# Kernel tuning notes

Measured on AMD Instinct MI355X. Metric: run time of the kernel, lower is better.

The kernel has to match this reference:

```python
import jax, jax.numpy as jnp
import numpy as np

B_SZ, L, D_MODEL = 2, 1024, 1024
EXPAND, D_STATE, D_CONV = 2, 16, 4
D_INNER = D_MODEL * EXPAND
DT_RANK = max(D_MODEL // 16, 1)


def setup_inputs() -> dict:
    key = jax.random.key(0)
    ks = jax.random.split(key, 9)
    s = 0.02
    x = jax.random.normal(ks[0], (B_SZ, L, D_MODEL), jnp.float32)
    W_in = jax.random.normal(ks[1], (2 * D_INNER, D_MODEL), jnp.float32) * s
    conv_w = jax.random.normal(ks[2], (D_INNER, D_CONV), jnp.float32) * 0.1
    conv_b = jax.random.normal(ks[3], (D_INNER,), jnp.float32) * 0.01
    W_x = jax.random.normal(ks[4], (DT_RANK + 2 * D_STATE, D_INNER), jnp.float32) * s
    W_dt = jax.random.normal(ks[5], (D_INNER, DT_RANK), jnp.float32) * s
    b_dt = jax.random.normal(ks[6], (D_INNER,), jnp.float32) * 0.01
    A_log = jnp.log(jnp.broadcast_to(jnp.arange(1, D_STATE + 1, dtype=jnp.float32), (D_INNER, D_STATE)))
    D_param = jnp.ones((D_INNER,), jnp.float32)
    W_out = jax.random.normal(ks[7], (D_MODEL, D_INNER), jnp.float32) * s
    return {"x": x, "W_in": W_in, "conv_w": conv_w, "conv_b": conv_b,
            "W_x": W_x, "W_dt": W_dt, "b_dt": b_dt, "A_log": A_log,
            "D_param": D_param, "W_out": W_out}


def _mamba_fwd(x, W_in, conv_w, conv_b, W_x, W_dt, b_dt, A_log, D_param, W_out):
    # in-proj and gate split
    xz = jnp.einsum("bld,ed->ble", x, W_in)            # (B, L, 2*d_inner)
    x_ssm, z = jnp.split(xz, 2, axis=-1)
    # causal depthwise 1D conv (left pad d_conv-1 == torch pad-both + [:L])
    xc = x_ssm.transpose(0, 2, 1)                        # (B, d_inner, L)
    xc = jax.lax.conv_general_dilated(
        xc, conv_w[:, None, :], window_strides=(1,),
        padding=[(D_CONV - 1, 0)], feature_group_count=D_INNER,
        dimension_numbers=("NCH", "OIH", "NCH"))
    xc = xc + conv_b[None, :, None]
    x_ssm = jax.nn.silu(xc.transpose(0, 2, 1))           # (B, L, d_inner)
    # input-dependent dt, B, C
    dbc = jnp.einsum("bld,ed->ble", x_ssm, W_x)
    dt, B_sel, C_sel = jnp.split(dbc, [DT_RANK, DT_RANK + D_STATE], axis=-1)
    delta = jax.nn.softplus(jnp.einsum("blr,dr->bld", dt, W_dt) + b_dt)
    A = -jnp.exp(A_log)                                  # (d_inner, d_state)
    # discretization
    deltaA = jnp.exp(delta[..., None] * A)               # (B, L, d_inner, d_state)
    dBu = delta[..., None] * B_sel[:, :, None, :] * x_ssm[..., None]
    # linear recurrence h_t = deltaA_t * h_{t-1} + dBu_t via associative scan
    def comb(e1, e2):
        a1, b1 = e1
        a2, b2 = e2
        return (a1 * a2, a2 * b1 + b2)
    _, h = jax.lax.associative_scan(comb, (deltaA, dBu), axis=1)
    y = jnp.sum(h * C_sel[:, :, None, :], axis=-1)       # (B, L, d_inner)
    y = y + x_ssm * D_param
    y = y * jax.nn.silu(z)
    return jnp.einsum("ble,de->bld", y, W_out)


def reference(x, W_in, conv_w, conv_b, W_x, W_dt, b_dt, A_log, D_param, W_out):
    return _mamba_fwd(x, W_in, conv_w, conv_b, W_x, W_dt, b_dt, A_log, D_param, W_out)
```

## Files before the change

kernel.cpp:

```cpp
#include <hip/hip_runtime.h>
#include <hip/hip_bf16.h>

#define B_SZ   2
#define SEQ    1024
#define DMODEL 1024
#define DINNER 2048
#define DSTATE 16
#define DCONV  4
#define DTRANK 64
#define BLROWS (B_SZ*SEQ)
#define NCHUNK 32
#define TCHUNK (SEQ/NCHUNK)
#define NSLICE 16
#define LOG2E 1.44269504088896f

using floatx4 = __attribute__((ext_vector_type(4))) float;
using short8  = __attribute__((ext_vector_type(8))) short;
using us8     = __attribute__((ext_vector_type(8))) unsigned short;
using us4     = __attribute__((ext_vector_type(4))) unsigned short;

__device__ __forceinline__ float softplus_f(float x) {
    return fmaxf(x, 0.f) + log1pf(__expf(-fabsf(x)));
}
__device__ __forceinline__ float silu_f(float x) {
    return x / (1.f + __expf(-x));
}
__device__ __forceinline__ short bfs(float x) {
    union { __hip_bfloat16 h; short s; } u;
    u.h = __float2bfloat16(x);
    return u.s;
}
__device__ __forceinline__ float b2f(unsigned short s) {
    union { float f; unsigned u; } x;
    x.u = ((unsigned)s) << 16;
    return x.f;
}
__device__ __forceinline__ void gld16(const void* g, void* l) {
    __builtin_amdgcn_global_load_lds((const __attribute__((address_space(1))) void*)g,
                                     (__attribute__((address_space(3))) void*)l,
                                     16, 0, 0);
}
__device__ __forceinline__ void cast8(const float* src, unsigned short* dst, int i) {
    const float* p = src + (size_t)i*8;
    float4 a = *(const float4*)p, b = *(const float4*)(p+4);
    us8 o;
    o[0]=(unsigned short)bfs(a.x); o[1]=(unsigned short)bfs(a.y);
    o[2]=(unsigned short)bfs(a.z); o[3]=(unsigned short)bfs(a.w);
    o[4]=(unsigned short)bfs(b.x); o[5]=(unsigned short)bfs(b.y);
    o[6]=(unsigned short)bfs(b.z); o[7]=(unsigned short)bfs(b.w);
    *(us8*)(dst + (size_t)i*8) = o;
}

#define G0 (BLROWS*DMODEL/8)
#define G1 (2*DINNER*DMODEL/8)
#define G2 (96*DINNER/8)
#define G3 (DINNER*DTRANK/8)
#define G4 (DMODEL*DINNER/8)
#define GTOT (G0+G1+G2+G3+G4)
__global__ __launch_bounds__(256)
void init_kernel(const float* __restrict__ x, const float* __restrict__ W_in,
                 const float* __restrict__ W_x, const float* __restrict__ W_dt,
                 const float* __restrict__ W_out,
                 unsigned short* xH, unsigned short* WinH, unsigned short* WxH,
                 unsigned short* WdtH, unsigned short* WoutH)
{
    int i = blockIdx.x*256 + threadIdx.x;
    if (i < G0) { cast8(x, xH, i); return; }            i -= G0;
    if (i < G1) { cast8(W_in, WinH, i); return; }       i -= G1;
    if (i < G2) { cast8(W_x, WxH, i); return; }         i -= G2;
    if (i < G3) { cast8(W_dt, WdtH, i); return; }       i -= G3;
    if (i < G4) { cast8(W_out, WoutH, i); }
}

template<int TM, int TN, int EPI, bool NGUARD>
__global__ __launch_bounds__(256)
void gemm_tn(const __hip_bfloat16* __restrict__ Ag, const __hip_bfloat16* __restrict__ Bg,
             int M, int N, int K, int kslice,
             float* __restrict__ outF,
             __hip_bfloat16* __restrict__ outH,
             __hip_bfloat16* __restrict__ outH2,
             const float* __restrict__ bias)
{
    constexpr int AG  = TM/64;
    constexpr int EB  = TN/64;
    constexpr int MF  = TM/32;
    constexpr int NF  = TN/32;
    constexpr int SM_SZ = 2*TM*32 + 2*TN*32;
    __shared__ short smem[SM_SZ];
    auto As = (short(*)[TM*32])smem;
    auto Bs = (short(*)[TN*32])(smem + 2*TM*32);

    const int tid  = threadIdx.x;
    const int lane = tid & 63, wave = tid >> 6;
    const int bm0  = blockIdx.x * TM;
    const int bn0  = blockIdx.y * TN;
    const int kbeg = blockIdx.z * kslice;
    const int kend = kbeg + kslice;
    const int wrow = (wave >> 1) * (TM/2), wcol = (wave & 1) * (TN/2);
    const int lrow = lane & 15, quad = lane >> 4;

    const int srow = wave*16 + (lane >> 2);
    const int scol = (lane & 3) * 8;

    const __hip_bfloat16* ga0 = Ag + (size_t)(bm0 + srow)*K      + scol;
    const __hip_bfloat16* ga1 = (AG > 1) ? Ag + (size_t)(bm0 + srow + 64)*K + scol : nullptr;
    const __hip_bfloat16* gb0 = Bg + (size_t)(bn0 + srow)*K      + scol;
    const __hip_bfloat16* gb1 = (EB > 1) ? Bg + (size_t)(bn0 + srow + 64)*K + scol : nullptr;
    const bool b0ok = !NGUARD || (bn0 + wave*16) < N;
    const bool b1ok = (EB > 1) && (!NGUARD || (bn0 + wave*16 + 64) < N);

    auto stage = [&](int c, int k0) {
        gld16(ga0 + k0, &As[c][(wave*16)*32]);
        if (AG > 1) gld16(ga1 + k0, &As[c][(wave*16 + 64)*32]);
        if (b0ok) gld16(gb0 + k0, &Bs[c][(wave*16)*32]);
        if (EB > 1 && b1ok) gld16(gb1 + k0, &Bs[c][(wave*16 + 64)*32]);
    };

    floatx4 acc[MF][NF] = {};

    stage(0, kbeg);
    __syncthreads();
    int cur = 0;
    for (int k0 = kbeg; k0 < kend; k0 += 32) {
        if (k0 + 32 < kend) stage(cur ^ 1, k0 + 32);
        short8 af[MF], bf[NF];
        #pragma unroll
        for (int i = 0; i < MF; i++)
            af[i] = *(const short8*)&As[cur][(wrow + i*16 + lrow)*32 + quad*8];
        #pragma unroll
        for (int j = 0; j < NF; j++)
            bf[j] = *(const short8*)&Bs[cur][(wcol + j*16 + lrow)*32 + quad*8];
        #pragma unroll
        for (int i = 0; i < MF; i++)
            #pragma unroll
            for (int j = 0; j < NF; j++)
                acc[i][j] = __builtin_amdgcn_mfma_f32_16x16x32_bf16(af[i], bf[j], acc[i][j], 0, 0, 0);
        __syncthreads();
        cur ^= 1;
    }

    const int rq = quad * 4;
    if constexpr (EPI == 8) {
        constexpr int TSTR = TM + 8;
        static_assert(TN*TSTR <= SM_SZ, "transpose buffer fits");
        short* t = smem;
        #pragma unroll
        for (int i = 0; i < MF; i++) {
            #pragma unroll
            for (int j = 0; j < NF; j++) {
                int cl = wcol + j*16 + lrow;
                int rl = wrow + i*16 + rq;
                us4 pk;
                #pragma unroll
                for (int r = 0; r < 4; r++)
                    pk[r] = (unsigned short)bfs(softplus_f(acc[i][j][r] + bias[bn0 + cl]));
                *(us4*)&t[cl*TSTR + rl] = pk;
            }
        }
        __syncthreads();
        const int bb = bm0 >> 10, lb = bm0 & (SEQ-1);
        constexpr int CPR  = TM/8;
        constexpr int ITER = (TM*TN)/(256*8);
        #pragma unroll
        for (int it = 0; it < ITER; ++it) {
            int idx = it*256 + tid;
            int dl = idx / CPR, lc = (idx % CPR)*8;
            us8 v = *(const us8*)&t[dl*TSTR + lc];
            *(us8*)((unsigned short*)outH + ((size_t)bb*DINNER + bn0 + dl)*SEQ + lb + lc) = v;
        }
    } else {
        #pragma unroll
        for (int i = 0; i < MF; i++) {
            #pragma unroll
            for (int j = 0; j < NF; j++) {
                int col = bn0 + wcol + j*16 + lrow;
                if (NGUARD && col >= N) continue;
                #pragma unroll
                for (int r = 0; r < 4; r++) {
                    int row = bm0 + wrow + i*16 + rq + r;
                    float v = acc[i][j][r];
                    if constexpr (EPI == 5) {
                        if (col < DINNER)
                            outH[(size_t)row*DINNER + col] = __float2bfloat16(v);
                        else
                            outH2[(size_t)row*DINNER + (col - DINNER)] = __float2bfloat16(v);
                    } else if constexpr (EPI == 9) {
                        outF[(size_t)blockIdx.z*M*N + (size_t)row*N + col] = v;
                    }
                }
            }
        }
    }
}

__global__ __launch_bounds__(192)
void dbc_reduce_kernel(const float* __restrict__ part, float* __restrict__ dbc,
                       __hip_bfloat16* __restrict__ dtH)
{
    const int tid = threadIdx.x;
    const int r2  = (tid >= 96) ? 1 : 0;
    const int col = tid - 96*r2;
    const int row = blockIdx.x*2 + r2;
    const size_t idx = (size_t)row*96 + col;
    float s = 0.f;
    #pragma unroll
    for (int z = 0; z < NSLICE; z++)
        s += part[(size_t)z*(BLROWS*96) + idx];
    dbc[idx] = s;
    if (col < DTRANK)
        dtH[(size_t)row*DTRANK + col] = __float2bfloat16(s);
}

__global__ __launch_bounds__(256)
void conv_transpose_kernel(const unsigned short* __restrict__ xbufN,
                           const float* __restrict__ cw,
                           const float* __restrict__ cb,
                           unsigned short* __restrict__ xsN,
                           unsigned short* __restrict__ xsT)
{
    __shared__ unsigned short t[67*68];
    __shared__ unsigned short t2[64*68];
    const int tid = threadIdx.x;
    const int l0 = blockIdx.x * 64, d0 = blockIdx.y * 64, b = blockIdx.z;

    const int lc4 = (tid & 15) * 4;
    for (int r = tid >> 4; r < 67; r += 16) {
        int lg = l0 - 3 + r;
        us4 v = {0,0,0,0};
        if (lg >= 0)
            v = *(const us4*)&xbufN[((size_t)(b*SEQ + lg))*DINNER + d0 + lc4];
        *(us4*)&t[r*68 + lc4] = v;
    }
    __syncthreads();

    const int dd = tid & 63;
    float4 w4 = *(const float4*)&cw[(d0 + dd)*4];
    float  bb = cb[d0 + dd];
    #pragma unroll 4
    for (int rr = tid >> 6; rr < 64; rr += 4) {
        float acc = bb;
        acc += w4.x * b2f(t[(rr+0)*68 + dd]);
        acc += w4.y * b2f(t[(rr+1)*68 + dd]);
        acc += w4.z * b2f(t[(rr+2)*68 + dd]);
        acc += w4.w * b2f(t[(rr+3)*68 + dd]);
        unsigned short h = (unsigned short)bfs(silu_f(acc));
        t2[rr*68 + dd] = h;
        xsN[((size_t)(b*SEQ + l0 + rr))*DINNER + d0 + dd] = h;
    }
    __syncthreads();

    const int dr = tid >> 4, lc = tid & 15;
    #pragma unroll
    for (int i = 0; i < 4; i++) {
        int dT = dr + i*16;
        us4 w;
        #pragma unroll
        for (int j = 0; j < 4; j++)
            w[j] = t2[(lc*4 + j)*68 + dT];
        *(us4*)&xsT[((size_t)b*DINNER + d0 + dT)*SEQ + l0 + lc*4] = w;
    }
}

__global__ __launch_bounds__(256)
void scan_pass1(const unsigned short* __restrict__ deT,
                const unsigned short* __restrict__ xsT,
                const float* __restrict__ dbc,
                const float* __restrict__ A_log,
                float* __restrict__ Bc, float* __restrict__ sde)
{
    const int tid = threadIdx.x;
    const int blk = blockIdx.x;
    const int dg  = blk & 7;
    const int c   = (blk >> 3) & (NCHUNK-1);
    const int b   = blk >> 8;
    const int d   = dg*256 + tid;

    float An[16];
    bool okv = true;
    #pragma unroll
    for (int n = 0; n < 16; n++) {
        An[n] = -__expf(A_log[d*DSTATE + n]) * LOG2E;
        okv = okv && (fabsf(An[n] + (float)(n+1)*LOG2E) < 2e-3f*(float)(n+1));
    }
    const bool fast = __all((int)okv);

    size_t rowT = ((size_t)b*DINNER + d)*SEQ;
    const float* brow = dbc + (size_t)b*SEQ*96 + (size_t)(c*TCHUNK)*96 + DTRANK;

    float h[16];
    #pragma unroll
    for (int n = 0; n < 16; n++) h[n] = 0.f;
    float s = 0.f;

    if (fast) {
        for (int t8 = 0; t8 < TCHUNK/8; ++t8) {
            int l0 = c*TCHUNK + t8*8;
            us8 de8 = *(const us8*)&deT[rowT + l0];
            us8 u8  = *(const us8*)&xsT[rowT + l0];
            #pragma unroll
            for (int j2 = 0; j2 < 8; j2++) {
                const float* br = brow + (size_t)(t8*8 + j2)*96;
                float de = b2f(de8[j2]);
                float du = de * b2f(u8[j2]);
                float r  = exp2f(de * (-LOG2E));
                float e  = r;
                #pragma unroll
                for (int n = 0; n < 16; n++) {
                    h[n] = e*h[n] + du*br[n];
                    e *= r;
                }
                s += de;
            }
        }
    } else {
        for (int t8 = 0; t8 < TCHUNK/8; ++t8) {
            int l0 = c*TCHUNK + t8*8;
            us8 de8 = *(const us8*)&deT[rowT + l0];
            us8 u8  = *(const us8*)&xsT[rowT + l0];
            #pragma unroll
            for (int j2 = 0; j2 < 8; j2++) {
                const float* br = brow + (size_t)(t8*8 + j2)*96;
                float de = b2f(de8[j2]);
                float du = de * b2f(u8[j2]);
                #pragma unroll
                for (int n = 0; n < 16; n++)
                    h[n] = exp2f(de*An[n])*h[n] + du*br[n];
                s += de;
            }
        }
    }

    size_t ci = (size_t)(b*NCHUNK + c)*DINNER + d;
    #pragma unroll
    for (int n = 0; n < 16; n += 4) {
        float4 v; v.x = h[n]; v.y = h[n+1]; v.z = h[n+2]; v.w = h[n+3];
        *(float4*)&Bc[ci*16 + n] = v;
    }
    sde[ci] = s;
}

__global__ __launch_bounds__(256)
void scan_pass2(float* __restrict__ Bc, const float* __restrict__ sde,
                const float* __restrict__ A_log)
{
    const int tid = threadIdx.x;
    const int n   = tid & 15, dl = tid >> 4;
    const int blk = blockIdx.x;
    const int dg  = blk & 127, b = blk >> 7;
    const int d   = dg*16 + dl;
    const float An = -__expf(A_log[d*DSTATE + n]) * LOG2E;

    float H = 0.f;
    for (int c = 0; c < NCHUNK; ++c) {
        size_t ci = (size_t)(b*NCHUNK + c)*DINNER + d;
        float bc = Bc[ci*16 + n];
        Bc[ci*16 + n] = H;
        H = exp2f(An*sde[ci])*H + bc;
    }
}

__global__ __launch_bounds__(256)
void scan_pass3(const unsigned short* __restrict__ deT,
                const unsigned short* __restrict__ xsT,
                const float* __restrict__ dbc,
                const float* __restrict__ A_log,
                const float* __restrict__ Dp,
                const float* __restrict__ Hinit,
                const unsigned short* __restrict__ zN,
                __hip_bfloat16* __restrict__ yN)
{
    const int tid = threadIdx.x;
    const int blk = blockIdx.x;
    const int dg  = blk & 7;
    const int c   = (blk >> 3) & (NCHUNK-1);
    const int b   = blk >> 8;
    const int d   = dg*256 + tid;

    float An[16];
    bool okv = true;
    #pragma unroll
    for (int n = 0; n < 16; n++) {
        An[n] = -__expf(A_log[d*DSTATE + n]) * LOG2E;
        okv = okv && (fabsf(An[n] + (float)(n+1)*LOG2E) < 2e-3f*(float)(n+1));
    }
    const bool fast = __all((int)okv);
    const float Dd = Dp[d];

    size_t rowT  = ((size_t)b*DINNER + d)*SEQ;
    size_t baseN = (size_t)b*SEQ*DINNER + d;
    const float* brow = dbc + (size_t)b*SEQ*96 + (size_t)(c*TCHUNK)*96 + DTRANK;

    size_t ci = (size_t)(b*NCHUNK + c)*DINNER + d;
    float h[16];
    #pragma unroll
    for (int n = 0; n < 16; n += 4) {
        float4 v = *(const float4*)&Hinit[ci*16 + n];
        h[n] = v.x; h[n+1] = v.y; h[n+2] = v.z; h[n+3] = v.w;
    }

    if (fast) {
        for (int t8 = 0; t8 < TCHUNK/8; ++t8) {
            int l0 = c*TCHUNK + t8*8;
            us8 de8 = *(const us8*)&deT[rowT + l0];
            us8 u8  = *(const us8*)&xsT[rowT + l0];
            #pragma unroll
            for (int j2 = 0; j2 < 8; j2++) {
                int l = l0 + j2;
                const float* br = brow + (size_t)(t8*8 + j2)*96;
                float de = b2f(de8[j2]);
                float u  = b2f(u8[j2]);
                float du = de * u;
                float r  = exp2f(de * (-LOG2E));
                float e  = r, cc = 0.f;
                #pragma unroll
                for (int n = 0; n < 16; n++) {
                    h[n] = e*h[n] + du*br[n];
                    cc  += h[n]*br[DSTATE + n];
                    e   *= r;
                }
                float zv = silu_f(b2f(zN[baseN + (size_t)l*DINNER]));
                yN[baseN + (size_t)l*DINNER] = __float2bfloat16((cc + u*Dd) * zv);
            }
        }
    } else {
        for (int t8 = 0; t8 < TCHUNK/8; ++t8) {
            int l0 = c*TCHUNK + t8*8;
            us8 de8 = *(const us8*)&deT[rowT + l0];
            us8 u8  = *(const us8*)&xsT[rowT + l0];
            #pragma unroll
            for (int j2 = 0; j2 < 8; j2++) {
                int l = l0 + j2;
                const float* br = brow + (size_t)(t8*8 + j2)*96;
                float de = b2f(de8[j2]);
                float u  = b2f(u8[j2]);
                float du = de * u;
                float cc = 0.f;
                #pragma unroll
                for (int n = 0; n < 16; n++) {
                    h[n] = exp2f(de*An[n])*h[n] + du*br[n];
                    cc  += h[n]*br[DSTATE + n];
                }
                float zv = silu_f(b2f(zN[baseN + (size_t)l*DINNER]));
                yN[baseN + (size_t)l*DINNER] = __float2bfloat16((cc + u*Dd) * zv);
            }
        }
    }
}

__global__ __launch_bounds__(256)
void zero_out_kernel(float* out, int n) {
    int i = blockIdx.x * 256 + threadIdx.x;
    if (i < n) out[i] = 0.f;
}

extern "C" void kernel_launch(void* const* d_in, const int* in_sizes, int n_in,
                              void* d_out, int out_size, void* d_ws, size_t ws_size,
                              hipStream_t stream) {
    const float* x      = (const float*)d_in[0];
    const float* W_in   = (const float*)d_in[1];
    const float* conv_w = (const float*)d_in[2];
    const float* conv_b = (const float*)d_in[3];
    const float* W_x    = (const float*)d_in[4];
    const float* W_dt   = (const float*)d_in[5];
    const float* b_dt   = (const float*)d_in[6];
    const float* A_log  = (const float*)d_in[7];
    const float* D_par  = (const float*)d_in[8];
    const float* W_out  = (const float*)d_in[9];

    size_t szBig = (size_t)BLROWS * DINNER * 2;
    size_t szBc  = (size_t)B_SZ * NCHUNK * DINNER * DSTATE * 4;
    size_t need  = 5*szBig
                 + (size_t)BLROWS*96*4
                 + (size_t)NSLICE*BLROWS*96*4
                 + (size_t)BLROWS*DTRANK*2
                 + szBc + (size_t)B_SZ*NCHUNK*DINNER*4
                 + (size_t)BLROWS*DMODEL*2
                 + (size_t)2*DINNER*DMODEL*2
                 + (size_t)128*DINNER*2
                 + (size_t)DINNER*DTRANK*2
                 + (size_t)DMODEL*DINNER*2;

    if (ws_size < need) {
        zero_out_kernel<<<(out_size + 255)/256, 256, 0, stream>>>((float*)d_out, out_size);
        return;
    }

    char* w = (char*)d_ws;
    __hip_bfloat16* xbufN = (__hip_bfloat16*)w;  w += szBig;
    __hip_bfloat16* zbufN = (__hip_bfloat16*)w;  w += szBig;
    __hip_bfloat16* xsN   = (__hip_bfloat16*)w;  w += szBig;
    __hip_bfloat16* xsT   = (__hip_bfloat16*)w;  w += szBig;
    __hip_bfloat16* deT   = (__hip_bfloat16*)w;  w += szBig;
    float*          dbc   = (float*)w;           w += (size_t)BLROWS * 96 * 4;
    float*          dbcP  = (float*)w;           w += (size_t)NSLICE * BLROWS * 96 * 4;
    __hip_bfloat16* dtH   = (__hip_bfloat16*)w;  w += (size_t)BLROWS * DTRANK * 2;
    float*          Bc    = (float*)w;           w += szBc;
    float*          sde   = (float*)w;           w += (size_t)B_SZ * NCHUNK * DINNER * 4;
    __hip_bfloat16* xH    = (__hip_bfloat16*)w;  w += (size_t)BLROWS*DMODEL*2;
    __hip_bfloat16* WinH  = (__hip_bfloat16*)w;  w += (size_t)2*DINNER*DMODEL*2;
    __hip_bfloat16* WxH   = (__hip_bfloat16*)w;  w += (size_t)128*DINNER*2;
    __hip_bfloat16* WdtH  = (__hip_bfloat16*)w;  w += (size_t)DINNER*DTRANK*2;
    __hip_bfloat16* WoutH = (__hip_bfloat16*)w;  w += (size_t)DMODEL*DINNER*2;
    __hip_bfloat16* yN    = xsN;

    init_kernel<<<GTOT/256, 256, 0, stream>>>(x, W_in, W_x, W_dt, W_out,
        (unsigned short*)xH, (unsigned short*)WinH, (unsigned short*)WxH,
        (unsigned short*)WdtH, (unsigned short*)WoutH);

    gemm_tn<128,128,5,false><<<dim3(BLROWS/128, (2*DINNER)/128, 1), 256, 0, stream>>>(
        xH, WinH, BLROWS, 2*DINNER, DMODEL, DMODEL, nullptr, xbufN, zbufN, nullptr);

    conv_transpose_kernel<<<dim3(SEQ/64, DINNER/64, B_SZ), 256, 0, stream>>>(
        (const unsigned short*)xbufN, conv_w, conv_b,
        (unsigned short*)xsN, (unsigned short*)xsT);

    gemm_tn<128,64,9,true><<<dim3(BLROWS/128, 2, NSLICE), 256, 0, stream>>>(
        xsN, WxH, BLROWS, 96, DINNER, DINNER/NSLICE, dbcP, nullptr, nullptr, nullptr);
    dbc_reduce_kernel<<<BLROWS/2, 192, 0, stream>>>(dbcP, dbc, dtH);

    gemm_tn<64,64,8,false><<<dim3(BLROWS/64, DINNER/64, 1), 256, 0, stream>>>(
        dtH, WdtH, BLROWS, DINNER, DTRANK, DTRANK, nullptr, deT, nullptr, b_dt);

    scan_pass1<<<B_SZ*NCHUNK*8, 256, 0, stream>>>((const unsigned short*)deT,
        (const unsigned short*)xsT, dbc, A_log, Bc, sde);
    scan_pass2<<<B_SZ*128, 256, 0, stream>>>(Bc, sde, A_log);
    scan_pass3<<<B_SZ*NCHUNK*8, 256, 0, stream>>>((const unsigned short*)deT,
        (const unsigned short*)xsT, dbc, A_log, D_par, Bc,
        (const unsigned short*)zbufN, yN);

    gemm_tn<64,64,9,false><<<dim3(BLROWS/64, DMODEL/64, 1), 256, 0, stream>>>(
        yN, WoutH, BLROWS, DMODEL, DINNER, DINNER, (float*)d_out, nullptr, nullptr, nullptr);
}
```

Measured before the change: 215.2 us.

## Interleave delta and conv outputs in 8-step groups and shorten decay power chain

The transposed delta and conv-output buffers change from a per-channel row layout (d, L) to a grouped layout (L/8, d, 8). Consecutive threads, one per channel, now read adjacent 16-byte chunks in the scan kernels, so those loads coalesce instead of striding by SEQ elements. The producers (GEMM epilogue and conv kernel) write the new layout, and the conv kernel moves to 8-wide stores. The serial e*=r decay chain is also replaced by a log-depth power tree to cut dependency latency, at the cost of a few more registers.

Result: no change. 216.4 us (+0.6%).

```diff
diff --git a/kernel.cpp b/kernel.cpp
--- a/kernel.cpp
+++ b/kernel.cpp
@@ -40,6 +40,13 @@
                                      (__attribute__((address_space(3))) void*)l,
                                      16, 0, 0);
 }
+__device__ __forceinline__ void pow_chain(float r, float* e) {
+    float r2 = r*r, r4 = r2*r2, r8 = r4*r4;
+    e[0] = r;      e[1] = r2;     e[2] = r*r2;   e[3] = r4;
+    e[4] = r*r4;   e[5] = r2*r4;  e[6] = e[2]*r4; e[7] = r8;
+    e[8] = r*r8;   e[9] = r2*r8;  e[10] = e[2]*r8; e[11] = r4*r8;
+    e[12] = e[4]*r8; e[13] = e[5]*r8; e[14] = e[6]*r8; e[15] = r8*r8;
+}
 __device__ __forceinline__ void cast8(const float* src, unsigned short* dst, int i) {
     const float* p = src + (size_t)i*8;
     float4 a = *(const float4*)p, b = *(const float4*)(p+4);
@@ -159,14 +166,16 @@
         }
         __syncthreads();
         const int bb = bm0 >> 10, lb = bm0 & (SEQ-1);
-        constexpr int CPR  = TM/8;
-        constexpr int ITER = (TM*TN)/(256*8);
+        constexpr int NGR  = (TM/8)*TN;
+        constexpr int ITER = NGR/256;
         #pragma unroll
         for (int it = 0; it < ITER; ++it) {
-            int idx = it*256 + tid;
-            int dl = idx / CPR, lc = (idx % CPR)*8;
-            us8 v = *(const us8*)&t[dl*TSTR + lc];
-            *(us8*)((unsigned short*)outH + ((size_t)bb*DINNER + bn0 + dl)*SEQ + lb + lc) = v;
+            int g   = it*256 + tid;
+            int dd  = g % TN;
+            int lch = g / TN;
+            us8 v = *(const us8*)&t[dd*TSTR + lch*8];
+            size_t gr = ((size_t)bb*(SEQ>>3) + (lb>>3) + lch)*DINNER + (bn0 + dd);
+            *(us8*)((unsigned short*)outH + gr*8) = v;
         }
     } else {
         #pragma unroll
@@ -249,15 +258,17 @@
     }
     __syncthreads();
 
-    const int dr = tid >> 4, lc = tid & 15;
-    #pragma unroll
-    for (int i = 0; i < 4; i++) {
-        int dT = dr + i*16;
-        us4 w;
-        #pragma unroll
-        for (int j = 0; j < 4; j++)
-            w[j] = t2[(lc*4 + j)*68 + dT];
-        *(us4*)&xsT[((size_t)b*DINNER + d0 + dT)*SEQ + l0 + lc*4] = w;
+    #pragma unroll
+    for (int it = 0; it < 2; ++it) {
+        int g   = it*256 + tid;
+        int dT  = g & 63;
+        int lch = g >> 6;
+        us8 v;
+        #pragma unroll
+        for (int j = 0; j < 8; j++)
+            v[j] = t2[(lch*8 + j)*68 + dT];
+        size_t gr = ((size_t)b*(SEQ>>3) + (l0>>3) + lch)*DINNER + d0 + dT;
+        *(us8*)&xsT[gr*8] = v;
     }
 }
 
@@ -284,7 +295,8 @@
     }
     const bool fast = __all((int)okv);
 
-    size_t rowT = ((size_t)b*DINNER + d)*SEQ;
+    const us8* de8p = (const us8*)deT;
+    const us8* u8p  = (const us8*)xsT;
     const float* brow = dbc + (size_t)b*SEQ*96 + (size_t)(c*TCHUNK)*96 + DTRANK;
 
     float h[16];
@@ -294,29 +306,28 @@
 
     if (fast) {
         for (int t8 = 0; t8 < TCHUNK/8; ++t8) {
-            int l0 = c*TCHUNK + t8*8;
-            us8 de8 = *(const us8*)&deT[rowT + l0];
-            us8 u8  = *(const us8*)&xsT[rowT + l0];
+            size_t gi = ((size_t)b*(SEQ>>3) + c*(TCHUNK>>3) + t8)*(size_t)DINNER + d;
+            us8 de8 = de8p[gi];
+            us8 u8  = u8p[gi];
             #pragma unroll
             for (int j2 = 0; j2 < 8; j2++) {
                 const float* br = brow + (size_t)(t8*8 + j2)*96;
                 float de = b2f(de8[j2]);
                 float du = de * b2f(u8[j2]);
                 float r  = exp2f(de * (-LOG2E));
-                float e  = r;
+                float e[16];
+                pow_chain(r, e);
                 #pragma unroll
-                for (int n = 0; n < 16; n++) {
-                    h[n] = e*h[n] + du*br[n];
-                    e *= r;
-                }
+                for (int n = 0; n < 16; n++)
+                    h[n] = e[n]*h[n] + du*br[n];
                 s += de;
             }
         }
     } else {
         for (int t8 = 0; t8 < TCHUNK/8; ++t8) {
-            int l0 = c*TCHUNK + t8*8;
-            us8 de8 = *(const us8*)&deT[rowT + l0];
-            us8 u8  = *(const us8*)&xsT[rowT + l0];
+            size_t gi = ((size_t)b*(SEQ>>3) + c*(TCHUNK>>3) + t8)*(size_t)DINNER + d;
+            us8 de8 = de8p[gi];
+            us8 u8  = u8p[gi];
             #pragma unroll
             for (int j2 = 0; j2 < 8; j2++) {
                 const float* br = brow + (size_t)(t8*8 + j2)*96;
@@ -386,7 +397,8 @@
     const bool fast = __all((int)okv);
     const float Dd = Dp[d];
 
-    size_t rowT  = ((size_t)b*DINNER + d)*SEQ;
+    const us8* de8p = (const us8*)deT;
+    const us8* u8p  = (const us8*)xsT;
     size_t baseN = (size_t)b*SEQ*DINNER + d;
     const float* brow = dbc + (size_t)b*SEQ*96 + (size_t)(c*TCHUNK)*96 + DTRANK;
 
@@ -400,23 +412,24 @@
 
     if (fast) {
         for (int t8 = 0; t8 < TCHUNK/8; ++t8) {
-            int l0 = c*TCHUNK + t8*8;
-            us8 de8 = *(const us8*)&deT[rowT + l0];
-            us8 u8  = *(const us8*)&xsT[rowT + l0];
+            size_t gi = ((size_t)b*(SEQ>>3) + c*(TCHUNK>>3) + t8)*(size_t)DINNER + d;
+            us8 de8 = de8p[gi];
+            us8 u8  = u8p[gi];
             #pragma unroll
             for (int j2 = 0; j2 < 8; j2++) {
-                int l = l0 + j2;
+                int l = c*TCHUNK + t8*8 + j2;
                 const float* br = brow + (size_t)(t8*8 + j2)*96;
                 float de = b2f(de8[j2]);
                 float u  = b2f(u8[j2]);
                 float du = de * u;
                 float r  = exp2f(de * (-LOG2E));
-                float e  = r, cc = 0.f;
+                float e[16];
+                pow_chain(r, e);
+                float cc = 0.f;
                 #pragma unroll
                 for (int n = 0; n < 16; n++) {
-                    h[n] = e*h[n] + du*br[n];
+                    h[n] = e[n]*h[n] + du*br[n];
                     cc  += h[n]*br[DSTATE + n];
-                    e   *= r;
                 }
                 float zv = silu_f(b2f(zN[baseN + (size_t)l*DINNER]));
                 yN[baseN + (size_t)l*DINNER] = __float2bfloat16((cc + u*Dd) * zv);
@@ -424,12 +437,12 @@
         }
     } else {
         for (int t8 = 0; t8 < TCHUNK/8; ++t8) {
-            int l0 = c*TCHUNK + t8*8;
-            us8 de8 = *(const us8*)&deT[rowT + l0];
-            us8 u8  = *(const us8*)&xsT[rowT + l0];
+            size_t gi = ((size_t)b*(SEQ>>3) + c*(TCHUNK>>3) + t8)*(size_t)DINNER + d;
+            us8 de8 = de8p[gi];
+            us8 u8  = u8p[gi];
             #pragma unroll
             for (int j2 = 0; j2 < 8; j2++) {
-                int l = l0 + j2;
+                int l = c*TCHUNK + t8*8 + j2;
                 const float* br = brow + (size_t)(t8*8 + j2)*96;
                 float de = b2f(de8[j2]);
                 float u  = b2f(u8[j2]);
```
